# Kernel optimization log

Hardware: AMD Instinct MI355X
Metric: run time of the kernel (lower is better)

The kernel has to match this reference:

```python
import jax, jax.numpy as jnp
import numpy as np

EPS = 1e-5


def setup_inputs() -> dict:
    key = jax.random.key(0)
    k1, k2, k3, k4, k5 = jax.random.split(key, 5)
    B, C, F, O = 32, 64, 16384, 128
    x = jax.random.normal(k1, (B, C, F), dtype=jnp.float32)
    adj = jax.random.randint(k2, (B, F, 4), 0, F, dtype=jnp.int64)
    # Conv1d(C, O, kernel_size=2, stride=2): weight [O, C, 2], bias [O]
    W = jax.random.normal(k3, (O, C, 2), dtype=jnp.float32) * (1.0 / np.sqrt(2 * C))
    b = jax.random.normal(k4, (O,), dtype=jnp.float32) * 0.01
    gamma = jnp.ones((O,), dtype=jnp.float32)
    beta_bn = jnp.zeros((O,), dtype=jnp.float32)
    return {"x": x, "adj": adj, "W": W, "b": b, "gamma": gamma, "beta_bn": beta_bn}


def reference(x, adj, W, b, gamma, beta_bn):
    B, C, F = x.shape
    xt = jnp.transpose(x, (0, 2, 1))                      # [B, F, C]
    # per-batch neighbor gather: re[b, f, k, :] = xt[b, adj[b, f, k], :]
    re = xt[jnp.arange(B)[:, None, None], adj]            # [B, F, 4, C]
    target = re[:, :, 0]                                  # [B, F, C] (alpha)
    neighbors = re[:, :, 1:]                              # [B, F, 3, C]
    beta_f = jnp.sum(jnp.abs(target[:, :, None, :] - neighbors), axis=2)  # [B, F, C]
    # Conv1d(k=2, s=2) over interleaved (alpha, beta) pairs == two matmuls
    y = (jnp.einsum("bfc,oc->bof", target, W[:, :, 0])
         + jnp.einsum("bfc,oc->bof", beta_f, W[:, :, 1])
         + b[None, :, None])                              # [B, O, F]
    # BatchNorm1d (training-mode batch stats over batch and length dims)
    mean = jnp.mean(y, axis=(0, 2), keepdims=True)
    var = jnp.var(y, axis=(0, 2), keepdims=True)
    y = (y - mean) * jax.lax.rsqrt(var + EPS)
    y = y * gamma[None, :, None] + beta_bn[None, :, None]
    return jax.nn.relu(y)
```

## Files before the change

kernel.cpp:

```cpp
#include <hip/hip_runtime.h>

#define B_DIM 32
#define C_DIM 64
#define F_DIM 16384
#define O_DIM 128
#define NBLK ((F_DIM / 64) * B_DIM)

typedef __attribute__((ext_vector_type(8))) short short8;
typedef __attribute__((ext_vector_type(4))) float f32x4;

__device__ __forceinline__ ushort f2bf(float f) {
    union { float f; uint u; } v; v.f = f;
    return (ushort)((v.u + 0x7FFFu + ((v.u >> 16) & 1u)) >> 16);
}
__device__ __forceinline__ float bflo(uint u) {
    union { uint u; float f; } v; v.u = u << 16; return v.f;
}
__device__ __forceinline__ float bfhi(uint u) {
    union { uint u; float f; } v; v.u = u & 0xFFFF0000u; return v.f;
}

__global__ __launch_bounds__(256) void k_transpose(const float* __restrict__ x,
                                                   ushort* __restrict__ xt,
                                                   const float* __restrict__ W,
                                                   ushort* __restrict__ Wtg) {
    __shared__ float tile[64][65];
    const int b  = blockIdx.y;
    const int f0 = blockIdx.x * 64;
    const int t  = threadIdx.x;
    const int fl = t & 63;
    const int q  = t >> 6;

    const float* xb = x + (size_t)b * C_DIM * F_DIM;
    #pragma unroll
    for (int i = 0; i < 16; ++i) {
        const int c = q + i * 4;
        tile[c][fl] = __builtin_nontemporal_load(&xb[(size_t)c * F_DIM + f0 + fl]);
    }

    if (blockIdx.x == 0 && blockIdx.y == 0 && t < 128) {
        const int o = t;
        #pragma unroll 8
        for (int c = 0; c < C_DIM; ++c) {
            Wtg[o * 128 + c]      = f2bf(W[o * 128 + c * 2]);
            Wtg[o * 128 + 64 + c] = f2bf(W[o * 128 + c * 2 + 1]);
        }
    }

    __syncthreads();

    const int f  = t >> 2;
    const int ch = t & 3;
    union { ushort s[16]; uint4 v[2]; } u;
    #pragma unroll
    for (int j = 0; j < 16; ++j)
        u.s[j] = f2bf(tile[ch * 16 + j][f]);
    ushort* dst = xt + ((size_t)b * F_DIM + f0 + f) * C_DIM + ch * 16;
    *(uint4*)(dst)     = u.v[0];
    *(uint4*)(dst + 8) = u.v[1];
}

template <int MODE>
__global__ __launch_bounds__(256, 3) void k_compute_t(const ushort* __restrict__ xt,
                                                      const int*    __restrict__ adj,
                                                      const ushort* __restrict__ Wtg,
                                                      const float*  __restrict__ bias,
                                                      const float*  __restrict__ ss,
                                                      float*        __restrict__ y,
                                                      float*        __restrict__ part) {
    __shared__ __align__(16) char Asm[64 * 256];
    __shared__ __align__(16) char Wsm[128 * 256];

    const int b  = blockIdx.y;
    const int f0 = blockIdx.x * 64;
    const int t  = threadIdx.x;

    const int p  = t >> 2;
    const int ch = t & 3;
    const int4 a4 = ((const int4*)adj)[(size_t)b * F_DIM + f0 + p];
    const char* xb = (const char*)(xt + (size_t)b * F_DIM * C_DIM);
    const char* r0 = xb + (size_t)a4.x * 128 + ch * 32;
    const char* r1 = xb + (size_t)a4.y * 128 + ch * 32;
    const char* r2 = xb + (size_t)a4.z * 128 + ch * 32;
    const char* r3 = xb + (size_t)a4.w * 128 + ch * 32;
    uint4 g[8];
    g[0] = *(const uint4*)(r0);  g[1] = *(const uint4*)(r0 + 16);
    g[2] = *(const uint4*)(r1);  g[3] = *(const uint4*)(r1 + 16);
    g[4] = *(const uint4*)(r2);  g[5] = *(const uint4*)(r2 + 16);
    g[6] = *(const uint4*)(r3);  g[7] = *(const uint4*)(r3 + 16);

    {
        const uint4* src = (const uint4*)Wtg;
        #pragma unroll
        for (int j = 0; j < 8; ++j) {
            const int fb    = t * 128 + j * 16;
            const int o     = fb >> 8;
            const int inner = fb & 255;
            *(uint4*)(Wsm + (o << 8) + (inner ^ ((o & 7) << 4))) = src[fb >> 4];
        }
    }

    {
        const int sw = (p & 7) << 4;
        char* Arow = Asm + p * 256;
        #pragma unroll
        for (int h = 0; h < 2; ++h) {
            const uint4 t0 = g[h], n1 = g[2 + h], n2 = g[4 + h], n3 = g[6 + h];
            *(uint4*)(Arow + ((ch * 32 + h * 16) ^ sw)) = t0;
            const uint tu[4] = { t0.x, t0.y, t0.z, t0.w };
            const uint au[4] = { n1.x, n1.y, n1.z, n1.w };
            const uint bu[4] = { n2.x, n2.y, n2.z, n2.w };
            const uint cu[4] = { n3.x, n3.y, n3.z, n3.w };
            uint bt[4];
            #pragma unroll
            for (int qq = 0; qq < 4; ++qq) {
                const float tl = bflo(tu[qq]), th = bfhi(tu[qq]);
                const float lo = fabsf(tl - bflo(au[qq])) + fabsf(tl - bflo(bu[qq])) + fabsf(tl - bflo(cu[qq]));
                const float hi = fabsf(th - bfhi(au[qq])) + fabsf(th - bfhi(bu[qq])) + fabsf(th - bfhi(cu[qq]));
                bt[qq] = (uint)f2bf(lo) | ((uint)f2bf(hi) << 16);
            }
            *(uint4*)(Arow + ((128 + ch * 32 + h * 16) ^ sw)) =
                make_uint4(bt[0], bt[1], bt[2], bt[3]);
        }
    }

    __syncthreads();

    const int w     = t >> 6;
    const int l     = t & 63;
    const int col16 = l & 15;
    const int gg    = l >> 4;
    const int swl   = (l & 7) << 4;

    f32x4 acc[8];
    #pragma unroll
    for (int s = 0; s < 8; ++s) {
        const float bv = bias[s * 16 + col16];
        acc[s] = (f32x4){ bv, bv, bv, bv };
    }

    const char* ArowR = Asm + (w * 16 + col16) * 256;
    #pragma unroll
    for (int kk = 0; kk < 4; ++kk) {
        const int koff = kk * 64 + gg * 16;
        const short8 af = *(const short8*)(ArowR + (koff ^ swl));
        #pragma unroll
        for (int s = 0; s < 8; ++s) {
            const short8 bf = *(const short8*)(Wsm + (s * 16 + col16) * 256 + (koff ^ swl));
            acc[s] = __builtin_amdgcn_mfma_f32_16x16x32_bf16(af, bf, acc[s], 0, 0, 0);
        }
    }

    if (MODE == 0) {
        __shared__ float sm_s[4][128];
        __shared__ float sm_q[4][128];
        #pragma unroll
        for (int s = 0; s < 8; ++s) {
            float ps = acc[s].x + acc[s].y + acc[s].z + acc[s].w;
            float pq = acc[s].x * acc[s].x + acc[s].y * acc[s].y
                     + acc[s].z * acc[s].z + acc[s].w * acc[s].w;
            ps += __shfl_xor(ps, 16, 64);  pq += __shfl_xor(pq, 16, 64);
            ps += __shfl_xor(ps, 32, 64);  pq += __shfl_xor(pq, 32, 64);
            if (gg == 0) {
                sm_s[w][s * 16 + col16] = ps;
                sm_q[w][s * 16 + col16] = pq;
            }
        }
        __syncthreads();
        if (t < 128) {
            const float a = sm_s[0][t] + sm_s[1][t] + sm_s[2][t] + sm_s[3][t];
            const float c = sm_q[0][t] + sm_q[1][t] + sm_q[2][t] + sm_q[3][t];
            const int blk = blockIdx.y * gridDim.x + blockIdx.x;
            part[(size_t)t * NBLK + blk]         = a;
            part[(size_t)(128 + t) * NBLK + blk] = c;
        }
    } else {
        const int fbase = f0 + w * 16 + gg * 4;
        #pragma unroll
        for (int s = 0; s < 8; ++s) {
            const int o = s * 16 + col16;
            const float sc = ss[o];
            const float sh = ss[O_DIM + o];
            f32x4 v = acc[s];
            v.x = fmaxf(fmaf(v.x, sc, sh), 0.f);
            v.y = fmaxf(fmaf(v.y, sc, sh), 0.f);
            v.z = fmaxf(fmaf(v.z, sc, sh), 0.f);
            v.w = fmaxf(fmaf(v.w, sc, sh), 0.f);
            __builtin_nontemporal_store(v, (f32x4*)(y + ((size_t)b * O_DIM + o) * F_DIM + fbase));
        }
    }
}

__global__ __launch_bounds__(256) void k_reduce_finalize(const float* __restrict__ part,
                                                         const float* __restrict__ gamma,
                                                         const float* __restrict__ beta_bn,
                                                         float* __restrict__ ss) {
    const int o = blockIdx.x;
    const int t = threadIdx.x;
    const float4* p1 = (const float4*)(part + (size_t)o * NBLK);
    const float4* p2 = (const float4*)(part + (size_t)(128 + o) * NBLK);
    float s = 0.f, q = 0.f;
    for (int i = t; i < NBLK / 4; i += 256) {
        const float4 v = p1[i];
        s += v.x + v.y + v.z + v.w;
        const float4 u = p2[i];
        q += u.x + u.y + u.z + u.w;
    }
    #pragma unroll
    for (int off = 32; off > 0; off >>= 1) {
        s += __shfl_down(s, off, 64);
        q += __shfl_down(q, off, 64);
    }
    __shared__ float ls[8];
    const int wid = t >> 6, lane = t & 63;
    if (lane == 0) { ls[wid] = s; ls[4 + wid] = q; }
    __syncthreads();
    if (t == 0) {
        const float ts = ls[0] + ls[1] + ls[2] + ls[3];
        const float tq = ls[4] + ls[5] + ls[6] + ls[7];
        const float n    = (float)B_DIM * (float)F_DIM;
        const float mean = ts / n;
        const float var  = tq / n - mean * mean;
        const float sc   = gamma[o] * rsqrtf(var + 1e-5f);
        ss[o]         = sc;
        ss[O_DIM + o] = beta_bn[o] - mean * sc;
    }
}

__global__ __launch_bounds__(256) void k_compute_slow(const float* __restrict__ xsrc,
                                                      const int*   __restrict__ adj,
                                                      const float* __restrict__ W,
                                                      const float* __restrict__ bias,
                                                      float*       __restrict__ y) {
    const int b = blockIdx.y;
    const int f = blockIdx.x * 256 + threadIdx.x;
    const int4 a = ((const int4*)adj)[(size_t)b * F_DIM + f];
    float tg[64], bt[64];
    const float* base = xsrc + (size_t)b * C_DIM * F_DIM;
    #pragma unroll
    for (int c = 0; c < 64; ++c) {
        const float tv = base[(size_t)c * F_DIM + a.x];
        const float n1 = base[(size_t)c * F_DIM + a.y];
        const float n2 = base[(size_t)c * F_DIM + a.z];
        const float n3 = base[(size_t)c * F_DIM + a.w];
        tg[c] = tv;
        bt[c] = fabsf(tv - n1) + fabsf(tv - n2) + fabsf(tv - n3);
    }
    float* yb = y + (size_t)b * O_DIM * F_DIM + f;
    const float2* W2 = (const float2*)W;
    #pragma unroll 4
    for (int o = 0; o < O_DIM; ++o) {
        float acc = bias[o];
        #pragma unroll
        for (int c = 0; c < 64; ++c) {
            const float2 wv = W2[o * 64 + c];
            acc = fmaf(tg[c], wv.x, fmaf(bt[c], wv.y, acc));
        }
        yb[(size_t)o * F_DIM] = acc;
    }
}

__global__ __launch_bounds__(256) void k_stats(const float* __restrict__ y,
                                               float* __restrict__ stats) {
    const int o = blockIdx.x;
    const int b = blockIdx.y;
    const float4* row = (const float4*)(y + ((size_t)b * O_DIM + o) * F_DIM);
    float s = 0.f, s2 = 0.f;
    for (int i = threadIdx.x; i < F_DIM / 4; i += 256) {
        const float4 v = row[i];
        s  += v.x + v.y + v.z + v.w;
        s2 += v.x * v.x + v.y * v.y + v.z * v.z + v.w * v.w;
    }
    #pragma unroll
    for (int off = 32; off > 0; off >>= 1) {
        s  += __shfl_down(s,  off, 64);
        s2 += __shfl_down(s2, off, 64);
    }
    __shared__ float ls[4], ls2[4];
    const int wid = threadIdx.x >> 6, lane = threadIdx.x & 63;
    if (lane == 0) { ls[wid] = s; ls2[wid] = s2; }
    __syncthreads();
    if (threadIdx.x == 0) {
        atomicAdd(&stats[o],         ls[0] + ls[1] + ls[2] + ls[3]);
        atomicAdd(&stats[O_DIM + o], ls2[0] + ls2[1] + ls2[2] + ls2[3]);
    }
}

__global__ void k_finalize(const float* __restrict__ stats,
                           const float* __restrict__ gamma,
                           const float* __restrict__ beta_bn,
                           float* __restrict__ ss) {
    const int o = threadIdx.x;
    if (o < O_DIM) {
        const float n    = (float)B_DIM * (float)F_DIM;
        const float mean = stats[o] / n;
        const float var  = stats[O_DIM + o] / n - mean * mean;
        const float sc   = gamma[o] * rsqrtf(var + 1e-5f);
        ss[o]         = sc;
        ss[O_DIM + o] = beta_bn[o] - mean * sc;
    }
}

__global__ __launch_bounds__(256) void k_norm(float* __restrict__ y,
                                              const float* __restrict__ ss) {
    const size_t n4 = (size_t)B_DIM * O_DIM * F_DIM / 4;
    const size_t stride = (size_t)gridDim.x * blockDim.x;
    float4* y4 = (float4*)y;
    for (size_t i = (size_t)blockIdx.x * blockDim.x + threadIdx.x; i < n4; i += stride) {
        const int o = (int)((i >> 12) & (O_DIM - 1));
        const float sc = ss[o];
        const float sh = ss[O_DIM + o];
        float4 v = y4[i];
        v.x = fmaxf(fmaf(v.x, sc, sh), 0.f);
        v.y = fmaxf(fmaf(v.y, sc, sh), 0.f);
        v.z = fmaxf(fmaf(v.z, sc, sh), 0.f);
        v.w = fmaxf(fmaf(v.w, sc, sh), 0.f);
        y4[i] = v;
    }
}

extern "C" void kernel_launch(void* const* d_in, const int* in_sizes, int n_in,
                              void* d_out, int out_size, void* d_ws, size_t ws_size,
                              hipStream_t stream) {
    const float* x       = (const float*)d_in[0];
    const int*   adj     = (const int*)  d_in[1];
    const float* W       = (const float*)d_in[2];
    const float* bias    = (const float*)d_in[3];
    const float* gamma   = (const float*)d_in[4];
    const float* beta_bn = (const float*)d_in[5];
    float* out = (float*)d_out;

    float*  stats = (float*)d_ws;
    float*  ss    = (float*)((char*)d_ws + 1024);
    ushort* Wtg   = (ushort*)((char*)d_ws + 4096);
    ushort* xt    = (ushort*)((char*)d_ws + 65536);
    float*  part  = (float*)((char*)d_ws + 65536 + (size_t)B_DIM * F_DIM * C_DIM * 2);
    const size_t need = 65536 + (size_t)B_DIM * F_DIM * C_DIM * 2
                      + (size_t)2 * O_DIM * NBLK * sizeof(float);

    if (ws_size >= need) {
        k_transpose<<<dim3(F_DIM / 64, B_DIM), 256, 0, stream>>>(x, xt, W, Wtg);
        k_compute_t<0><<<dim3(F_DIM / 64, B_DIM), 256, 0, stream>>>(xt, adj, Wtg, bias, nullptr, nullptr, part);
        k_reduce_finalize<<<O_DIM, 256, 0, stream>>>(part, gamma, beta_bn, ss);
        k_compute_t<1><<<dim3(F_DIM / 64, B_DIM), 256, 0, stream>>>(xt, adj, Wtg, bias, ss, out, nullptr);
    } else {
        hipMemsetAsync(stats, 0, 2 * O_DIM * sizeof(float), stream);
        k_compute_slow<<<dim3(F_DIM / 256, B_DIM), 256, 0, stream>>>(x, adj, W, bias, out);
        k_stats<<<dim3(O_DIM, B_DIM), 256, 0, stream>>>(out, stats);
        k_finalize<<<1, 128, 0, stream>>>(stats, gamma, beta_bn, ss);
        k_norm<<<2048, 256, 0, stream>>>(out, ss);
    }
}
```

Measured before the change: 205.2 us.

## Process four tiles per block with register-fed MFMA and prefetched gathers

Each compute block now handles four 64-row tiles instead of one. The weight matrix is staged into LDS once per four tiles, which amortises that load. The A operand is built directly in registers from the gathered rows, so the Asm LDS buffer, its stores and the extra barrier are gone. The gather for the next tile is issued before the current tile's MFMAs, giving a two-slot register prefetch. The cost is higher register pressure (two gather buffers plus accumulators under launch_bounds 256,3) and a quarter as many blocks, which could reduce occupancy or latency hiding.

New measurement: 417.6 us. +103.5%, slower.

```diff
diff --git a/kernel.cpp b/kernel.cpp
--- a/kernel.cpp
+++ b/kernel.cpp
@@ -4,7 +4,8 @@
 #define C_DIM 64
 #define F_DIM 16384
 #define O_DIM 128
-#define NBLK ((F_DIM / 64) * B_DIM)
+#define TPB   4
+#define NBLK2 ((F_DIM / 64 / TPB) * B_DIM)
 
 typedef __attribute__((ext_vector_type(8))) short short8;
 typedef __attribute__((ext_vector_type(4))) float f32x4;
@@ -18,6 +19,15 @@
 }
 __device__ __forceinline__ float bfhi(uint u) {
     union { uint u; float f; } v; v.u = u & 0xFFFF0000u; return v.f;
+}
+__device__ __forceinline__ uint beta_pair(uint tu, uint au, uint bu, uint cu) {
+    const float tl = bflo(tu), th = bfhi(tu);
+    const float lo = fabsf(tl - bflo(au)) + fabsf(tl - bflo(bu)) + fabsf(tl - bflo(cu));
+    const float hi = fabsf(th - bfhi(au)) + fabsf(th - bfhi(bu)) + fabsf(th - bfhi(cu));
+    return (uint)f2bf(lo) | ((uint)f2bf(hi) << 16);
+}
+__device__ __forceinline__ short8 as_s8(uint4 u) {
+    union { uint4 u; short8 s; } cv; cv.u = u; return cv.s;
 }
 
 __global__ __launch_bounds__(256) void k_transpose(const float* __restrict__ x,
@@ -68,26 +78,42 @@
                                                       const float*  __restrict__ ss,
                                                       float*        __restrict__ y,
                                                       float*        __restrict__ part) {
-    __shared__ __align__(16) char Asm[64 * 256];
     __shared__ __align__(16) char Wsm[128 * 256];
 
-    const int b  = blockIdx.y;
-    const int f0 = blockIdx.x * 64;
-    const int t  = threadIdx.x;
-
-    const int p  = t >> 2;
-    const int ch = t & 3;
-    const int4 a4 = ((const int4*)adj)[(size_t)b * F_DIM + f0 + p];
+    const int t     = threadIdx.x;
+    const int w     = t >> 6;
+    const int l     = t & 63;
+    const int col16 = l & 15;
+    const int g     = l >> 4;
+    const int co    = g * 16;
+
+    const int blk  = blockIdx.x;
+    const int ti0  = blk * TPB;
+    const int b    = ti0 >> 8;
+    const int frow = w * 16 + col16;
+
+    const int4* adjp = (const int4*)adj + (size_t)b * F_DIM;
+    int4 a4[TPB];
+    #pragma unroll
+    for (int i = 0; i < TPB; ++i)
+        a4[i] = adjp[((ti0 + i) & 255) * 64 + frow];
+
     const char* xb = (const char*)(xt + (size_t)b * F_DIM * C_DIM);
-    const char* r0 = xb + (size_t)a4.x * 128 + ch * 32;
-    const char* r1 = xb + (size_t)a4.y * 128 + ch * 32;
-    const char* r2 = xb + (size_t)a4.z * 128 + ch * 32;
-    const char* r3 = xb + (size_t)a4.w * 128 + ch * 32;
-    uint4 g[8];
-    g[0] = *(const uint4*)(r0);  g[1] = *(const uint4*)(r0 + 16);
-    g[2] = *(const uint4*)(r1);  g[3] = *(const uint4*)(r1 + 16);
-    g[4] = *(const uint4*)(r2);  g[5] = *(const uint4*)(r2 + 16);
-    g[6] = *(const uint4*)(r3);  g[7] = *(const uint4*)(r3 + 16);
+
+    uint4 gb[2][8];
+    #define ISSUE_GATHER(slot, a)                                              \
+        do {                                                                   \
+            gb[slot][0] = *(const uint4*)(xb + (size_t)(a).x * 128 + co);      \
+            gb[slot][1] = *(const uint4*)(xb + (size_t)(a).x * 128 + 64 + co); \
+            gb[slot][2] = *(const uint4*)(xb + (size_t)(a).y * 128 + co);      \
+            gb[slot][3] = *(const uint4*)(xb + (size_t)(a).y * 128 + 64 + co); \
+            gb[slot][4] = *(const uint4*)(xb + (size_t)(a).z * 128 + co);      \
+            gb[slot][5] = *(const uint4*)(xb + (size_t)(a).z * 128 + 64 + co); \
+            gb[slot][6] = *(const uint4*)(xb + (size_t)(a).w * 128 + co);      \
+            gb[slot][7] = *(const uint4*)(xb + (size_t)(a).w * 128 + 64 + co); \
+        } while (0)
+
+    ISSUE_GATHER(0, a4[0]);
 
     {
         const uint4* src = (const uint4*)Wtg;
@@ -99,94 +125,99 @@
             *(uint4*)(Wsm + (o << 8) + (inner ^ ((o & 7) << 4))) = src[fb >> 4];
         }
     }
-
-    {
-        const int sw = (p & 7) << 4;
-        char* Arow = Asm + p * 256;
-        #pragma unroll
-        for (int h = 0; h < 2; ++h) {
-            const uint4 t0 = g[h], n1 = g[2 + h], n2 = g[4 + h], n3 = g[6 + h];
-            *(uint4*)(Arow + ((ch * 32 + h * 16) ^ sw)) = t0;
-            const uint tu[4] = { t0.x, t0.y, t0.z, t0.w };
-            const uint au[4] = { n1.x, n1.y, n1.z, n1.w };
-            const uint bu[4] = { n2.x, n2.y, n2.z, n2.w };
-            const uint cu[4] = { n3.x, n3.y, n3.z, n3.w };
-            uint bt[4];
+    __syncthreads();
+
+    float ps[8], pq[8];
+    if (MODE == 0) {
+        #pragma unroll
+        for (int s = 0; s < 8; ++s) { ps[s] = 0.f; pq[s] = 0.f; }
+    }
+
+    const int swl = (col16 & 7) << 4;
+
+    #pragma unroll
+    for (int i = 0; i < TPB; ++i) {
+        if (i + 1 < TPB) ISSUE_GATHER((i + 1) & 1, a4[i + 1]);
+
+        short8 af[4];
+        af[0] = as_s8(gb[i & 1][0]);
+        af[1] = as_s8(gb[i & 1][1]);
+        {
+            const uint4 t0 = gb[i & 1][0], t1 = gb[i & 1][1];
+            const uint4 x1 = gb[i & 1][2], y1 = gb[i & 1][3];
+            const uint4 x2 = gb[i & 1][4], y2 = gb[i & 1][5];
+            const uint4 x3 = gb[i & 1][6], y3 = gb[i & 1][7];
+            af[2] = as_s8(make_uint4(beta_pair(t0.x, x1.x, x2.x, x3.x),
+                                     beta_pair(t0.y, x1.y, x2.y, x3.y),
+                                     beta_pair(t0.z, x1.z, x2.z, x3.z),
+                                     beta_pair(t0.w, x1.w, x2.w, x3.w)));
+            af[3] = as_s8(make_uint4(beta_pair(t1.x, y1.x, y2.x, y3.x),
+                                     beta_pair(t1.y, y1.y, y2.y, y3.y),
+                                     beta_pair(t1.z, y1.z, y2.z, y3.z),
+                                     beta_pair(t1.w, y1.w, y2.w, y3.w)));
+        }
+
+        f32x4 acc[8];
+        #pragma unroll
+        for (int s = 0; s < 8; ++s) {
+            const float bv = bias[s * 16 + col16];
+            acc[s] = (f32x4){ bv, bv, bv, bv };
+        }
+        #pragma unroll
+        for (int kk = 0; kk < 4; ++kk) {
             #pragma unroll
-            for (int qq = 0; qq < 4; ++qq) {
-                const float tl = bflo(tu[qq]), th = bfhi(tu[qq]);
-                const float lo = fabsf(tl - bflo(au[qq])) + fabsf(tl - bflo(bu[qq])) + fabsf(tl - bflo(cu[qq]));
-                const float hi = fabsf(th - bfhi(au[qq])) + fabsf(th - bfhi(bu[qq])) + fabsf(th - bfhi(cu[qq]));
-                bt[qq] = (uint)f2bf(lo) | ((uint)f2bf(hi) << 16);
+            for (int s = 0; s < 8; ++s) {
+                const short8 bf = *(const short8*)(Wsm + (s * 16 + col16) * 256
+                                                   + ((kk * 64 + g * 16) ^ swl));
+                acc[s] = __builtin_amdgcn_mfma_f32_16x16x32_bf16(af[kk], bf, acc[s], 0, 0, 0);
             }
-            *(uint4*)(Arow + ((128 + ch * 32 + h * 16) ^ sw)) =
-                make_uint4(bt[0], bt[1], bt[2], bt[3]);
-        }
-    }
-
-    __syncthreads();
-
-    const int w     = t >> 6;
-    const int l     = t & 63;
-    const int col16 = l & 15;
-    const int gg    = l >> 4;
-    const int swl   = (l & 7) << 4;
-
-    f32x4 acc[8];
-    #pragma unroll
-    for (int s = 0; s < 8; ++s) {
-        const float bv = bias[s * 16 + col16];
-        acc[s] = (f32x4){ bv, bv, bv, bv };
-    }
-
-    const char* ArowR = Asm + (w * 16 + col16) * 256;
-    #pragma unroll
-    for (int kk = 0; kk < 4; ++kk) {
-        const int koff = kk * 64 + gg * 16;
-        const short8 af = *(const short8*)(ArowR + (koff ^ swl));
-        #pragma unroll
-        for (int s = 0; s < 8; ++s) {
-            const short8 bf = *(const short8*)(Wsm + (s * 16 + col16) * 256 + (koff ^ swl));
-            acc[s] = __builtin_amdgcn_mfma_f32_16x16x32_bf16(af, bf, acc[s], 0, 0, 0);
-        }
-    }
+        }
+
+        if (MODE == 0) {
+            #pragma unroll
+            for (int s = 0; s < 8; ++s) {
+                ps[s] += acc[s].x + acc[s].y + acc[s].z + acc[s].w;
+                pq[s] += acc[s].x * acc[s].x + acc[s].y * acc[s].y
+                       + acc[s].z * acc[s].z + acc[s].w * acc[s].w;
+            }
+        } else {
+            const int f0    = ((ti0 + i) & 255) * 64;
+            const int fbase = f0 + w * 16 + g * 4;
+            #pragma unroll
+            for (int s = 0; s < 8; ++s) {
+                const int o = s * 16 + col16;
+                const float sc = ss[o];
+                const float sh = ss[O_DIM + o];
+                f32x4 v = acc[s];
+                v.x = fmaxf(fmaf(v.x, sc, sh), 0.f);
+                v.y = fmaxf(fmaf(v.y, sc, sh), 0.f);
+                v.z = fmaxf(fmaf(v.z, sc, sh), 0.f);
+                v.w = fmaxf(fmaf(v.w, sc, sh), 0.f);
+                __builtin_nontemporal_store(v, (f32x4*)(y + ((size_t)b * O_DIM + o) * F_DIM + fbase));
+            }
+        }
+    }
+    #undef ISSUE_GATHER
 
     if (MODE == 0) {
         __shared__ float sm_s[4][128];
         __shared__ float sm_q[4][128];
         #pragma unroll
         for (int s = 0; s < 8; ++s) {
-            float ps = acc[s].x + acc[s].y + acc[s].z + acc[s].w;
-            float pq = acc[s].x * acc[s].x + acc[s].y * acc[s].y
-                     + acc[s].z * acc[s].z + acc[s].w * acc[s].w;
-            ps += __shfl_xor(ps, 16, 64);  pq += __shfl_xor(pq, 16, 64);
-            ps += __shfl_xor(ps, 32, 64);  pq += __shfl_xor(pq, 32, 64);
-            if (gg == 0) {
-                sm_s[w][s * 16 + col16] = ps;
-                sm_q[w][s * 16 + col16] = pq;
+            float a = ps[s], c = pq[s];
+            a += __shfl_xor(a, 16, 64);  c += __shfl_xor(c, 16, 64);
+            a += __shfl_xor(a, 32, 64);  c += __shfl_xor(c, 32, 64);
+            if (g == 0) {
+                sm_s[w][s * 16 + col16] = a;
+                sm_q[w][s * 16 + col16] = c;
             }
         }
         __syncthreads();
         if (t < 128) {
             const float a = sm_s[0][t] + sm_s[1][t] + sm_s[2][t] + sm_s[3][t];
             const float c = sm_q[0][t] + sm_q[1][t] + sm_q[2][t] + sm_q[3][t];
-            const int blk = blockIdx.y * gridDim.x + blockIdx.x;
-            part[(size_t)t * NBLK + blk]         = a;
-            part[(size_t)(128 + t) * NBLK + blk] = c;
-        }
-    } else {
-        const int fbase = f0 + w * 16 + gg * 4;
-        #pragma unroll
-        for (int s = 0; s < 8; ++s) {
-            const int o = s * 16 + col16;
-            const float sc = ss[o];
-            const float sh = ss[O_DIM + o];
-            f32x4 v = acc[s];
-            v.x = fmaxf(fmaf(v.x, sc, sh), 0.f);
-            v.y = fmaxf(fmaf(v.y, sc, sh), 0.f);
-            v.z = fmaxf(fmaf(v.z, sc, sh), 0.f);
-            v.w = fmaxf(fmaf(v.w, sc, sh), 0.f);
-            __builtin_nontemporal_store(v, (f32x4*)(y + ((size_t)b * O_DIM + o) * F_DIM + fbase));
+            part[(size_t)t * NBLK2 + blk]         = a;
+            part[(size_t)(128 + t) * NBLK2 + blk] = c;
         }
     }
 }
@@ -197,10 +228,10 @@
                                                          float* __restrict__ ss) {
     const int o = blockIdx.x;
     const int t = threadIdx.x;
-    const float4* p1 = (const float4*)(part + (size_t)o * NBLK);
-    const float4* p2 = (const float4*)(part + (size_t)(128 + o) * NBLK);
+    const float4* p1 = (const float4*)(part + (size_t)o * NBLK2);
+    const float4* p2 = (const float4*)(part + (size_t)(128 + o) * NBLK2);
     float s = 0.f, q = 0.f;
-    for (int i = t; i < NBLK / 4; i += 256) {
+    for (int i = t; i < NBLK2 / 4; i += 256) {
         const float4 v = p1[i];
         s += v.x + v.y + v.z + v.w;
         const float4 u = p2[i];
@@ -336,13 +367,13 @@
     ushort* xt    = (ushort*)((char*)d_ws + 65536);
     float*  part  = (float*)((char*)d_ws + 65536 + (size_t)B_DIM * F_DIM * C_DIM * 2);
     const size_t need = 65536 + (size_t)B_DIM * F_DIM * C_DIM * 2
-                      + (size_t)2 * O_DIM * NBLK * sizeof(float);
+                      + (size_t)2 * O_DIM * NBLK2 * sizeof(float);
 
     if (ws_size >= need) {
         k_transpose<<<dim3(F_DIM / 64, B_DIM), 256, 0, stream>>>(x, xt, W, Wtg);
-        k_compute_t<0><<<dim3(F_DIM / 64, B_DIM), 256, 0, stream>>>(xt, adj, Wtg, bias, nullptr, nullptr, part);
+        k_compute_t<0><<<dim3(NBLK2), 256, 0, stream>>>(xt, adj, Wtg, bias, nullptr, nullptr, part);
         k_reduce_finalize<<<O_DIM, 256, 0, stream>>>(part, gamma, beta_bn, ss);
-        k_compute_t<1><<<dim3(F_DIM / 64, B_DIM), 256, 0, stream>>>(xt, adj, Wtg, bias, ss, out, nullptr);
+        k_compute_t<1><<<dim3(NBLK2), 256, 0, stream>>>(xt, adj, Wtg, bias, ss, out, nullptr);
     } else {
         hipMemsetAsync(stats, 0, 2 * O_DIM * sizeof(float), stream);
         k_compute_slow<<<dim3(F_DIM / 256, B_DIM), 256, 0, stream>>>(x, adj, W, bias, out);
```

## Store bf16 pre-norm output in first pass and normalize in separate elementwise kernel

Applied to the files above, without the earlier changes.

The first compute pass now also writes the pre-normalization activations as bf16 to workspace. A new elementwise kernel reads them back, applies the BN scale/shift and ReLU, and writes fp32 output. This replaces the second gather-plus-MFMA recompute pass. It adds a 128 MB bf16 write and read in exchange, and it rounds the output through bf16. The grid is also flattened to 1D with a batch-major block index.

Result: slower. 235.7 us (+14.9%).

```diff
diff --git a/kernel.cpp b/kernel.cpp
--- a/kernel.cpp
+++ b/kernel.cpp
@@ -67,13 +67,15 @@
                                                       const float*  __restrict__ bias,
                                                       const float*  __restrict__ ss,
                                                       float*        __restrict__ y,
+                                                      ushort*       __restrict__ ybf,
                                                       float*        __restrict__ part) {
     __shared__ __align__(16) char Asm[64 * 256];
     __shared__ __align__(16) char Wsm[128 * 256];
 
-    const int b  = blockIdx.y;
-    const int f0 = blockIdx.x * 64;
-    const int t  = threadIdx.x;
+    const int bid  = blockIdx.x;
+    const int b    = bid >> 8;
+    const int f0   = (bid & 255) * 64;
+    const int t    = threadIdx.x;
 
     const int p  = t >> 2;
     const int ch = t & 3;
@@ -92,8 +94,8 @@
     {
         const uint4* src = (const uint4*)Wtg;
         #pragma unroll
-        for (int j = 0; j < 8; ++j) {
-            const int fb    = t * 128 + j * 16;
+        for (int jj = 0; jj < 8; ++jj) {
+            const int fb    = t * 128 + jj * 16;
             const int o     = fb >> 8;
             const int inner = fb & 255;
             *(uint4*)(Wsm + (o << 8) + (inner ^ ((o & 7) << 4))) = src[fb >> 4];
@@ -151,7 +153,20 @@
         }
     }
 
-    if (MODE == 0) {
+    const int fbase = f0 + w * 16 + gg * 4;
+
+    if (MODE == 2) {
+        #pragma unroll
+        for (int s = 0; s < 8; ++s) {
+            const int o = s * 16 + col16;
+            uint2 pk;
+            pk.x = (uint)f2bf(acc[s].x) | ((uint)f2bf(acc[s].y) << 16);
+            pk.y = (uint)f2bf(acc[s].z) | ((uint)f2bf(acc[s].w) << 16);
+            *(uint2*)(ybf + ((size_t)b * O_DIM + o) * F_DIM + fbase) = pk;
+        }
+    }
+
+    if (MODE == 0 || MODE == 2) {
         __shared__ float sm_s[4][128];
         __shared__ float sm_q[4][128];
         #pragma unroll
@@ -170,12 +185,10 @@
         if (t < 128) {
             const float a = sm_s[0][t] + sm_s[1][t] + sm_s[2][t] + sm_s[3][t];
             const float c = sm_q[0][t] + sm_q[1][t] + sm_q[2][t] + sm_q[3][t];
-            const int blk = blockIdx.y * gridDim.x + blockIdx.x;
-            part[(size_t)t * NBLK + blk]         = a;
-            part[(size_t)(128 + t) * NBLK + blk] = c;
+            part[(size_t)t * NBLK + bid]         = a;
+            part[(size_t)(128 + t) * NBLK + bid] = c;
         }
     } else {
-        const int fbase = f0 + w * 16 + gg * 4;
         #pragma unroll
         for (int s = 0; s < 8; ++s) {
             const int o = s * 16 + col16;
@@ -224,6 +237,30 @@
         const float sc   = gamma[o] * rsqrtf(var + 1e-5f);
         ss[o]         = sc;
         ss[O_DIM + o] = beta_bn[o] - mean * sc;
+    }
+}
+
+__global__ __launch_bounds__(256) void k_norm_bf(const ushort* __restrict__ ybf,
+                                                 const float* __restrict__ ss,
+                                                 float* __restrict__ out) {
+    const size_t n8 = (size_t)B_DIM * O_DIM * F_DIM / 8;
+    const size_t stride = (size_t)gridDim.x * blockDim.x;
+    for (size_t i = (size_t)blockIdx.x * blockDim.x + threadIdx.x; i < n8; i += stride) {
+        const int o = (int)((i >> 11) & (O_DIM - 1));
+        const float sc = ss[o];
+        const float sh = ss[O_DIM + o];
+        const uint4 v = *(const uint4*)(ybf + i * 8);
+        f32x4 r0, r1;
+        r0.x = fmaxf(fmaf(bflo(v.x), sc, sh), 0.f);
+        r0.y = fmaxf(fmaf(bfhi(v.x), sc, sh), 0.f);
+        r0.z = fmaxf(fmaf(bflo(v.y), sc, sh), 0.f);
+        r0.w = fmaxf(fmaf(bfhi(v.y), sc, sh), 0.f);
+        r1.x = fmaxf(fmaf(bflo(v.z), sc, sh), 0.f);
+        r1.y = fmaxf(fmaf(bfhi(v.z), sc, sh), 0.f);
+        r1.z = fmaxf(fmaf(bflo(v.w), sc, sh), 0.f);
+        r1.w = fmaxf(fmaf(bfhi(v.w), sc, sh), 0.f);
+        __builtin_nontemporal_store(r0, (f32x4*)(out + i * 8));
+        __builtin_nontemporal_store(r1, (f32x4*)(out + i * 8 + 4));
     }
 }
 
@@ -330,19 +367,30 @@
     const float* beta_bn = (const float*)d_in[5];
     float* out = (float*)d_out;
 
+    const size_t XT_B   = (size_t)B_DIM * F_DIM * C_DIM * 2;
+    const size_t PART_B = (size_t)2 * O_DIM * NBLK * sizeof(float);
+    const size_t YBF_B  = (size_t)B_DIM * O_DIM * F_DIM * 2;
+
     float*  stats = (float*)d_ws;
     float*  ss    = (float*)((char*)d_ws + 1024);
     ushort* Wtg   = (ushort*)((char*)d_ws + 4096);
     ushort* xt    = (ushort*)((char*)d_ws + 65536);
-    float*  part  = (float*)((char*)d_ws + 65536 + (size_t)B_DIM * F_DIM * C_DIM * 2);
-    const size_t need = 65536 + (size_t)B_DIM * F_DIM * C_DIM * 2
-                      + (size_t)2 * O_DIM * NBLK * sizeof(float);
-
-    if (ws_size >= need) {
+    float*  part  = (float*)((char*)d_ws + 65536 + XT_B);
+    ushort* ybf   = (ushort*)((char*)d_ws + 65536 + XT_B + PART_B);
+
+    const size_t need_big = 65536 + XT_B + PART_B + YBF_B;
+    const size_t need_mid = 65536 + XT_B + PART_B;
+
+    if (ws_size >= need_big) {
         k_transpose<<<dim3(F_DIM / 64, B_DIM), 256, 0, stream>>>(x, xt, W, Wtg);
-        k_compute_t<0><<<dim3(F_DIM / 64, B_DIM), 256, 0, stream>>>(xt, adj, Wtg, bias, nullptr, nullptr, part);
+        k_compute_t<2><<<dim3(NBLK), 256, 0, stream>>>(xt, adj, Wtg, bias, nullptr, nullptr, ybf, part);
         k_reduce_finalize<<<O_DIM, 256, 0, stream>>>(part, gamma, beta_bn, ss);
-        k_compute_t<1><<<dim3(F_DIM / 64, B_DIM), 256, 0, stream>>>(xt, adj, Wtg, bias, ss, out, nullptr);
+        k_norm_bf<<<4096, 256, 0, stream>>>(ybf, ss, out);
+    } else if (ws_size >= need_mid) {
+        k_transpose<<<dim3(F_DIM / 64, B_DIM), 256, 0, stream>>>(x, xt, W, Wtg);
+        k_compute_t<0><<<dim3(NBLK), 256, 0, stream>>>(xt, adj, Wtg, bias, nullptr, nullptr, nullptr, part);
+        k_reduce_finalize<<<O_DIM, 256, 0, stream>>>(part, gamma, beta_bn, ss);
+        k_compute_t<1><<<dim3(NBLK), 256, 0, stream>>>(xt, adj, Wtg, bias, ss, out, nullptr, nullptr);
     } else {
         hipMemsetAsync(stats, 0, 2 * O_DIM * sizeof(float), stream);
         k_compute_slow<<<dim3(F_DIM / 256, B_DIM), 256, 0, stream>>>(x, adj, W, bias, out);
```
